# Kernel tuning notes

Measured on AMD Instinct MI355X. Metric: run time of the kernel, lower is better.

## Reference

```python
import jax, jax.numpy as jnp
import numpy as np

N_EMBD = 1024
N_HEAD = 16
HEAD_DIM = N_EMBD // N_HEAD


def setup_inputs() -> dict:
    key = jax.random.key(0)
    k1, k2, k3 = jax.random.split(key, 3)
    B, T, C = 2, 2048, N_EMBD
    x = jax.random.normal(k1, (B, T, C), dtype=jnp.float32)
    # torch nn.Linear(n_embd, 3*n_embd): weight [3C, C], bias [3C]
    W = jax.random.normal(k2, (3 * C, C), dtype=jnp.float32) * (1.0 / np.sqrt(C))
    b = jax.random.normal(k3, (3 * C,), dtype=jnp.float32) * 0.01
    return {"x": x, "W": W, "b": b}


def reference(x, W, b):
    B, T, C = x.shape
    H, D = N_HEAD, HEAD_DIM
    qkv = jnp.einsum('btc,oc->bto', x, W) + b          # [B,T,3C]
    q, k, v = jnp.split(qkv, 3, axis=2)
    # [B,H,T,D]
    q = q.reshape(B, T, H, D).transpose(0, 2, 1, 3)
    k = k.reshape(B, T, H, D).transpose(0, 2, 1, 3)
    v = v.reshape(B, T, H, D).transpose(0, 2, 1, 3)
    scale = 1.0 / np.sqrt(D).astype(np.float32)
    scores = jnp.einsum('bhid,bhjd->bhij', q, k) * scale   # [B,H,T,T]
    causal = jnp.tril(jnp.ones((T, T), dtype=bool))
    w = jnp.where(causal, jax.nn.relu(scores), 0.0)        # ReLU, no softmax
    y = jnp.einsum('bhij,bhjd->bhid', w, v)                # [B,H,T,D]
    return y.transpose(0, 2, 1, 3).reshape(B, T, C)
```

## Files before the change

### kernel.cpp

```cpp
#include <hip/hip_runtime.h>

typedef __bf16 bf16;
typedef __bf16 bf16x8 __attribute__((ext_vector_type(8)));
typedef float  f32x4  __attribute__((ext_vector_type(4)));

#define T_SEQ   2048
#define D_HEAD  64
#define NH      16
#define BH      32
#define C_EMB   1024
#define WS_STRIDE (BH * T_SEQ * D_HEAD)
#define XN (4096 * 1024)
#define WN (3072 * 1024)
#define WS_NEEDED ((size_t)(3 * WS_STRIDE + XN + WN) * 2)
#define CVT_GRID 3584

__device__ __forceinline__ bf16x8 cvt8(float4 a, float4 b) {
    bf16x8 r;
    r[0] = (__bf16)a.x; r[1] = (__bf16)a.y; r[2] = (__bf16)a.z; r[3] = (__bf16)a.w;
    r[4] = (__bf16)b.x; r[5] = (__bf16)b.y; r[6] = (__bf16)b.z; r[7] = (__bf16)b.w;
    return r;
}

__device__ __forceinline__ void gl_lds16(const bf16* g, bf16* l) {
    __builtin_amdgcn_global_load_lds(
        (const __attribute__((address_space(1))) unsigned int*)g,
        (__attribute__((address_space(3))) unsigned int*)l,
        16, 0, 0);
}

__device__ __forceinline__ unsigned pack_bf16(float a, float b) {
    union { __bf16 h[2]; unsigned u; } pk;
    pk.h[0] = (__bf16)a; pk.h[1] = (__bf16)b;
    return pk.u;
}

__global__ __launch_bounds__(256) void cvt_bf16(
    const float* __restrict__ x, const float* __restrict__ W,
    bf16* __restrict__ xb, bf16* __restrict__ wb)
{
    const int t = blockIdx.x * 256 + threadIdx.x;
    const float* src; bf16* dst; int base;
    if (t < XN / 8) { src = x; dst = xb; base = t * 8; }
    else           { src = W; dst = wb; base = (t - XN / 8) * 8; }
    float4 a = *(const float4*)(src + base);
    float4 b = *(const float4*)(src + base + 4);
    *(bf16x8*)(dst + base) = cvt8(a, b);
}

#define LDA(d, qi) {                                                          \
    const bf16* abase_ = Sh + (d)*16384 + (qi)*8192 + (wm*64 + l15)*64;       \
    _Pragma("unroll")                                                         \
    for (int ii_ = 0; ii_ < 4; ii_++) {                                       \
        _Pragma("unroll")                                                     \
        for (int dk_ = 0; dk_ < 2; dk_++)                                     \
            aF[ii_][dk_] = *(const bf16x8*)(abase_ + ii_*1024                 \
                                            + (((dk_*4 + l4) ^ k7) * 8));     \
    }                                                                         \
}

#define LDB(d, qj, bFv) {                                                     \
    const bf16* bbase_ = Sh + 32768 + (d)*16384 + (qj)*8192                   \
                         + (wn*32 + l15)*64;                                  \
    _Pragma("unroll")                                                         \
    for (int jj_ = 0; jj_ < 2; jj_++) {                                       \
        _Pragma("unroll")                                                     \
        for (int dk_ = 0; dk_ < 2; dk_++)                                     \
            bFv[jj_][dk_] = *(const bf16x8*)(bbase_ + jj_*1024                \
                                             + (((dk_*4 + l4) ^ k7) * 8));    \
    }                                                                         \
}

#define STA(d, qi, s, ko) gl_lds16(                                           \
    aSrc + (size_t)((qi)*64 + (s)*128) * 1024 + (ko),                         \
    Sh + (d)*16384 + (qi)*8192 + (s)*4096 + w*512)

#define STB(d, qj, s, ko) gl_lds16(                                           \
    bSrc + (size_t)((s)*128 + (qj)*32) * 1024 + (ko),                         \
    Sh + 32768 + (d)*16384 + (qj)*8192 + (s)*4096 + w*512)

#define MMAQ(qi, qj, bFv) {                                                   \
    __builtin_amdgcn_s_setprio(1);                                            \
    _Pragma("unroll")                                                         \
    for (int dk_ = 0; dk_ < 2; dk_++) {                                       \
        _Pragma("unroll")                                                     \
        for (int ii_ = 0; ii_ < 4; ii_++) {                                   \
            _Pragma("unroll")                                                 \
            for (int jj_ = 0; jj_ < 2; jj_++)                                 \
                acc[(qi)*4 + ii_][(qj)*2 + jj_] =                             \
                    __builtin_amdgcn_mfma_f32_16x16x32_bf16(                  \
                        aF[ii_][dk_], bFv[jj_][dk_],                          \
                        acc[(qi)*4 + ii_][(qj)*2 + jj_], 0, 0, 0);            \
        }                                                                     \
    }                                                                         \
    __builtin_amdgcn_s_setprio(0);                                            \
}

#define BAR   __builtin_amdgcn_s_barrier()
#define LGKM0 asm volatile("s_waitcnt lgkmcnt(0)" ::: "memory")

#define HALF(d, sk)                                                           \
                                                                      \
    LDA(d, 0) LDB(d, 0, bF0)                                                  \
    BAR; LGKM0;                                                               \
    MMAQ(0, 0, bF0)                                                           \
    BAR;                                                                      \
                                                                      \
    LDB(d, 1, bF1)                                                            \
    STA(d, 0, 0, sk); STA(d, 0, 1, sk); STB(d, 0, 0, sk); STB(d, 0, 1, sk);   \
    BAR; LGKM0;                                                               \
    MMAQ(0, 1, bF1)                                                           \
    BAR;                                                                      \
                                                                      \
    LDA(d, 1)                                                                 \
    STB(d, 1, 0, sk); STB(d, 1, 1, sk);                                       \
    BAR; LGKM0;                                                               \
    MMAQ(1, 0, bF0)                                                           \
    BAR;                                                                      \
                                                                      \
    STA(d, 1, 0, sk); STA(d, 1, 1, sk);                                       \
    BAR;                                                                      \
    MMAQ(1, 1, bF1)                                                           \
    asm volatile("s_waitcnt vmcnt(8)" ::: "memory");                          \
    BAR;

__global__ __launch_bounds__(512, 2) void qkv_gemm3(
    const bf16* __restrict__ xb, const bf16* __restrict__ wb,
    const float* __restrict__ bias, bf16* __restrict__ ws)
{
    __shared__ bf16 Sh[65536];

    const int tid  = threadIdx.x;
    const int lane = tid & 63;
    const int w    = tid >> 6;
    const int wm   = w >> 2, wn = w & 3;
    const int l15  = lane & 15, l4 = lane >> 4;
    const int k7   = l15 & 7;
    const int l8   = lane >> 3;
    const int csw  = (lane & 7) ^ l8;

    const int swz = (blockIdx.x & 7) * 24 + (blockIdx.x >> 3);
    const int bm  = swz / 12, bn = swz % 12;

    const bf16* aSrc = xb + (size_t)(bm * 256 + w * 8 + l8) * 1024 + csw * 8;
    const bf16* bSrc = wb + (size_t)(bn * 256 + (w >> 2) * 64 + (w & 3) * 8 + l8) * 1024
                          + csw * 8;

    f32x4 acc[8][4];
#pragma unroll
    for (int i = 0; i < 8; i++)
#pragma unroll
        for (int j = 0; j < 4; j++) acc[i][j] = (f32x4){0.f, 0.f, 0.f, 0.f};

    bf16x8 aF[4][2], bF0[2][2], bF1[2][2];

    STA(0,0,0,0);  STA(0,0,1,0);  STB(0,0,0,0);  STB(0,0,1,0);
    STB(0,1,0,0);  STB(0,1,1,0);  STA(0,1,0,0);  STA(0,1,1,0);
    STA(1,0,0,64); STA(1,0,1,64); STB(1,0,0,64); STB(1,0,1,64);
    STB(1,1,0,64); STB(1,1,1,64); STA(1,1,0,64); STA(1,1,1,64);
    asm volatile("s_waitcnt vmcnt(8)" ::: "memory");
    BAR;

    for (int it = 0; it < 8; ++it) {
        const int sk0 = (it < 7 ? (2 * it + 2) : 15) * 64;
        const int sk1 = (it < 7 ? (2 * it + 3) : 15) * 64;
        HALF(0, sk0)
        HALF(1, sk1)
    }
    asm volatile("s_waitcnt vmcnt(0)" ::: "memory");
    BAR;

    float bv[4];
#pragma unroll
    for (int j = 0; j < 4; j++) bv[j] = bias[bn * 256 + wn * 64 + j * 16 + l15];

    const int which = bn >> 2;
    const int h     = (bn & 3) * 4 + wn;
    const int bi    = bm >> 3;
    const int tBase = (bm & 7) * 256 + wm * 128;
    const float qs  = (which == 0) ? 0.125f : 1.0f;
    bf16* Wl = Sh + w * 8192;

    if (which < 2) {
#pragma unroll
        for (int i = 0; i < 8; i++)
#pragma unroll
            for (int j = 0; j < 4; j++)
#pragma unroll
                for (int r = 0; r < 4; r++) {
                    const int lm = i * 16 + l4 * 4 + r;
                    const int dd = j * 16 + l15;
                    const int cp = (dd >> 3) ^ (lm & 7);
                    Wl[lm * 64 + cp * 8 + (dd & 7)] =
                        (__bf16)((acc[i][j][r] + bv[j]) * qs);
                }
#pragma unroll
        for (int e = 0; e < 16; e++) {
            const int lm = e * 8 + l8;
            const int c  = lane & 7;
            bf16x8 v8 = *(const bf16x8*)&Wl[lm * 64 + ((c ^ (lm & 7)) * 8)];
            const int t = tBase + lm;
            *(bf16x8*)&ws[(size_t)which * WS_STRIDE
                          + ((size_t)(bi * NH + h) * T_SEQ + t) * D_HEAD + c * 8] = v8;
        }
    } else {
#pragma unroll
        for (int i = 0; i < 8; i++)
#pragma unroll
            for (int j = 0; j < 4; j++) {
                const int dd = j * 16 + l15;
#pragma unroll
                for (int p = 0; p < 2; p++) {
                    const int lm = i * 16 + l4 * 4 + 2 * p;
                    const int ch = lm >> 3;
                    const int cp = (ch & 8) | ((ch & 7) ^ (dd & 7));
                    *(unsigned*)&Wl[dd * 128 + cp * 8 + (lm & 7)] =
                        pack_bf16(acc[i][j][2 * p] + bv[j],
                                  acc[i][j][2 * p + 1] + bv[j]);
                }
            }
        bf16* vt = ws + 2 * (size_t)WS_STRIDE;
#pragma unroll
        for (int e = 0; e < 16; e++) {
            const int dd = e * 4 + l4;
            const int c  = l15;
            const int cp = (c & 8) | ((c & 7) ^ (dd & 7));
            bf16x8 v8 = *(const bf16x8*)&Wl[dd * 128 + cp * 8];
            *(bf16x8*)&vt[((size_t)(bi * NH + h) * D_HEAD + dd) * T_SEQ
                          + tBase + c * 8] = v8;
        }
    }
}

__global__ __launch_bounds__(256) void qkv_gemm(
    const float* __restrict__ x, const float* __restrict__ W,
    const float* __restrict__ bias, bf16* __restrict__ ws)
{
    __shared__ bf16 As[128 * 40];
    __shared__ bf16 Bs[128 * 40];

    const int tid  = threadIdx.x;
    const int lane = tid & 63;
    const int w    = tid >> 6;
    const int wm   = w >> 1, wn = w & 1;
    const int l15  = lane & 15, l4 = lane >> 4;
    const int bm   = blockIdx.x / 24, bn = blockIdx.x % 24;

    const int srow = tid >> 1;
    const int scol = (tid & 1) * 16;
    const float* xg = x + (size_t)(bm * 128 + srow) * 1024 + scol;
    const float* wg = W + (size_t)(bn * 128 + srow) * 1024 + scol;
    bf16* asw = &As[srow * 40 + scol];
    bf16* bsw = &Bs[srow * 40 + scol];

    f32x4 acc[4][4];
#pragma unroll
    for (int i = 0; i < 4; i++)
#pragma unroll
        for (int j = 0; j < 4; j++) acc[i][j] = (f32x4){0.f, 0.f, 0.f, 0.f};

    float bv[4];
#pragma unroll
    for (int j = 0; j < 4; j++) bv[j] = bias[bn * 128 + wn * 64 + j * 16 + l15];

    for (int kk = 0; kk < 32; ++kk) {
        const float* xp = xg + kk * 32;
        const float* wp = wg + kk * 32;
        float4 a0 = *(const float4*)(xp + 0);
        float4 a1 = *(const float4*)(xp + 4);
        float4 a2 = *(const float4*)(xp + 8);
        float4 a3 = *(const float4*)(xp + 12);
        float4 b0 = *(const float4*)(wp + 0);
        float4 b1 = *(const float4*)(wp + 4);
        float4 b2 = *(const float4*)(wp + 8);
        float4 b3 = *(const float4*)(wp + 12);

        __syncthreads();
        *(bf16x8*)(asw + 0) = cvt8(a0, a1);
        *(bf16x8*)(asw + 8) = cvt8(a2, a3);
        *(bf16x8*)(bsw + 0) = cvt8(b0, b1);
        *(bf16x8*)(bsw + 8) = cvt8(b2, b3);
        __syncthreads();

        bf16x8 aF[4], bF[4];
#pragma unroll
        for (int s = 0; s < 4; s++) {
            aF[s] = *(const bf16x8*)&As[(wm * 64 + s * 16 + l15) * 40 + l4 * 8];
            bF[s] = *(const bf16x8*)&Bs[(wn * 64 + s * 16 + l15) * 40 + l4 * 8];
        }
#pragma unroll
        for (int i = 0; i < 4; i++)
#pragma unroll
            for (int j = 0; j < 4; j++)
                acc[i][j] = __builtin_amdgcn_mfma_f32_16x16x32_bf16(
                    aF[i], bF[j], acc[i][j], 0, 0, 0);
    }

#pragma unroll
    for (int i = 0; i < 4; i++) {
#pragma unroll
        for (int j = 0; j < 4; j++) {
            const int n     = bn * 128 + wn * 64 + j * 16 + l15;
            const int which = n >> 10;
            const int cc    = n & 1023;
            const int h     = cc >> 6, d = cc & 63;
            const float qs  = (which == 0) ? 0.125f : 1.0f;
#pragma unroll
            for (int r = 0; r < 4; r++) {
                const int m  = bm * 128 + wm * 64 + i * 16 + l4 * 4 + r;
                const int bi = m >> 11, t = m & 2047;
                const int bh = bi * NH + h;
                const float v = (acc[i][j][r] + bv[j]) * qs;
                size_t idx;
                if (which == 2)
                    idx = 2 * (size_t)WS_STRIDE + ((size_t)bh * D_HEAD + d) * T_SEQ + t;
                else
                    idx = (size_t)which * WS_STRIDE + ((size_t)bh * T_SEQ + t) * D_HEAD + d;
                ws[idx] = (__bf16)v;
            }
        }
    }
}

__global__ __launch_bounds__(256) void attn(
    const bf16* __restrict__ ws, float* __restrict__ out)
{
    __shared__ bf16 Ks[128 * 64];
    __shared__ bf16 Vts[64 * 128];

    const int tid  = threadIdx.x;
    const int lane = tid & 63;
    const int w    = tid >> 6;
    const int l15  = lane & 15, qd = lane >> 4;

    const int bh = blockIdx.x & 31;
    const int u  = blockIdx.x >> 5;
    const int qt = (u < 8) ? u : (23 - u);
    const int nj = qt + 1;
    const int qb = qt * 128;

    const bf16* qg = ws + (size_t)bh * (T_SEQ * D_HEAD);
    const bf16* kg = ws + WS_STRIDE + (size_t)bh * (T_SEQ * D_HEAD);
    const bf16* vt = ws + 2 * (size_t)WS_STRIDE + (size_t)bh * (D_HEAD * T_SEQ);
    const int b = bh >> 4, h = bh & 15;

    const int ksub = lane >> 3;
    const int kc   = lane & 7;
    const int vsub = qd;
    const int vc   = l15;

    bf16x8 qF[2][2];
#pragma unroll
    for (int sm = 0; sm < 2; sm++)
#pragma unroll
        for (int dk = 0; dk < 2; dk++)
            qF[sm][dk] = *(const bf16x8*)(qg
                + (qb + w * 32 + sm * 16 + l15) * 64 + dk * 32 + qd * 8);

    f32x4 o[2][4];
#pragma unroll
    for (int sm = 0; sm < 2; sm++)
#pragma unroll
        for (int sd = 0; sd < 4; sd++) o[sm][sd] = (f32x4){0.f, 0.f, 0.f, 0.f};

    for (int jt = 0; jt < nj; ++jt) {
        __syncthreads();
#pragma unroll
        for (int e = 0; e < 4; e++) {
            const int rb = w * 32 + e * 8;
            gl_lds16(kg + (size_t)(jt * 128 + rb + ksub) * 64 + ((kc ^ ksub) * 8),
                     &Ks[rb * 64]);
        }
#pragma unroll
        for (int e = 0; e < 4; e++) {
            const int rb = w * 16 + e * 4;
            const int sw = (rb & 12) + vsub;
            gl_lds16(vt + (size_t)(rb + vsub) * T_SEQ + jt * 128 + ((vc ^ sw) * 8),
                     &Vts[rb * 128]);
        }
        __syncthreads();

        const bool need_mask = (jt == nj - 1);
        unsigned PK[2][8][2];
#pragma unroll
        for (int kn = 0; kn < 8; kn++) {
            const int r7  = 4 * (kn & 1) + (l15 & 3);
            const int row = 32 * (kn >> 1) + 8 * (l15 >> 2) + r7;
            bf16x8 kf0 = *(const bf16x8*)&Ks[row * 64 + ((qd ^ r7) * 8)];
            bf16x8 kf1 = *(const bf16x8*)&Ks[row * 64 + (((4 + qd) ^ r7) * 8)];
            f32x4 s0 = {0.f, 0.f, 0.f, 0.f}, s1 = {0.f, 0.f, 0.f, 0.f};
            s0 = __builtin_amdgcn_mfma_f32_16x16x32_bf16(kf0, qF[0][0], s0, 0, 0, 0);
            s0 = __builtin_amdgcn_mfma_f32_16x16x32_bf16(kf1, qF[0][1], s0, 0, 0, 0);
            s1 = __builtin_amdgcn_mfma_f32_16x16x32_bf16(kf0, qF[1][0], s1, 0, 0, 0);
            s1 = __builtin_amdgcn_mfma_f32_16x16x32_bf16(kf1, qF[1][1], s1, 0, 0, 0);
            const int keyb = jt * 128 + 32 * (kn >> 1) + 8 * qd + 4 * (kn & 1);
#pragma unroll
            for (int sm = 0; sm < 2; sm++) {
                const f32x4 sv = sm ? s1 : s0;
                const int q = qb + w * 32 + sm * 16 + l15;
                float v[4];
#pragma unroll
                for (int r = 0; r < 4; r++) {
                    float val = fmaxf(sv[r], 0.f);
                    if (need_mask && q < keyb + r) val = 0.f;
                    v[r] = val;
                }
                PK[sm][kn][0] = pack_bf16(v[0], v[1]);
                PK[sm][kn][1] = pack_bf16(v[2], v[3]);
            }
        }

#pragma unroll
        for (int kk = 0; kk < 4; kk++) {
            bf16x8 pF[2];
#pragma unroll
            for (int sm = 0; sm < 2; sm++) {
                union { unsigned dw[4]; bf16x8 v; } uu;
                uu.dw[0] = PK[sm][2 * kk + 0][0];
                uu.dw[1] = PK[sm][2 * kk + 0][1];
                uu.dw[2] = PK[sm][2 * kk + 1][0];
                uu.dw[3] = PK[sm][2 * kk + 1][1];
                pF[sm] = uu.v;
            }
#pragma unroll
            for (int sd = 0; sd < 4; sd++) {
                bf16x8 vf = *(const bf16x8*)&Vts[(sd * 16 + l15) * 128
                                                 + (((kk * 4 + qd) ^ l15) * 8)];
                o[0][sd] = __builtin_amdgcn_mfma_f32_16x16x32_bf16(pF[0], vf, o[0][sd], 0, 0, 0);
                o[1][sd] = __builtin_amdgcn_mfma_f32_16x16x32_bf16(pF[1], vf, o[1][sd], 0, 0, 0);
            }
        }
    }

#pragma unroll
    for (int sm = 0; sm < 2; sm++)
#pragma unroll
        for (int sd = 0; sd < 4; sd++) {
            const int d = sd * 16 + l15;
#pragma unroll
            for (int r = 0; r < 4; r++) {
                const int t = qb + w * 32 + sm * 16 + qd * 4 + r;
                out[((size_t)b * T_SEQ + t) * C_EMB + h * 64 + d] = o[sm][sd][r];
            }
        }
}

extern "C" void kernel_launch(void* const* d_in, const int* in_sizes, int n_in,
                              void* d_out, int out_size, void* d_ws, size_t ws_size,
                              hipStream_t stream) {
    const float* x    = (const float*)d_in[0];
    const float* W    = (const float*)d_in[1];
    const float* bias = (const float*)d_in[2];
    float* out        = (float*)d_out;
    bf16*  ws         = (bf16*)d_ws;

    if (ws_size >= WS_NEEDED) {
        bf16* xb = ws + 3 * (size_t)WS_STRIDE;
        bf16* wb = xb + XN;
        cvt_bf16<<<dim3(CVT_GRID), dim3(256), 0, stream>>>(x, W, xb, wb);
        qkv_gemm3<<<dim3(192), dim3(512), 0, stream>>>(xb, wb, bias, ws);
    } else {
        qkv_gemm<<<dim3(768), dim3(256), 0, stream>>>(x, W, bias, ws);
    }
    attn<<<dim3(512), dim3(256), 0, stream>>>(ws, out);
}
```

Baseline: 148.1 us.

## Double-buffer K/V tiles in attention and raise MFMA wave priority

The attention kernel now keeps two LDS buffers for the K and V^T tiles and issues the direct-to-LDS loads for the next key tile before computing on the current one, using vmcnt waits and barriers. This overlaps global-memory latency with MFMA work instead of stalling at each iteration. It also wraps the MFMA sequences in s_setprio and moves the causal-mask check out of the unmasked path. LDS use doubles to 64 KB per block, which may lower occupancy. Correctness depends on the hand-written vmcnt(8) count matching the eight loads issued per stage.

```diff
diff --git a/kernel.cpp b/kernel.cpp
--- a/kernel.cpp
+++ b/kernel.cpp
@@ -322,11 +322,29 @@
     }
 }
 
+#define ASTAGE(jt_, p_) {                                                     \
+    _Pragma("unroll")                                                         \
+    for (int e_ = 0; e_ < 4; e_++) {                                          \
+        const int rb_ = w * 32 + e_ * 8;                                      \
+        gl_lds16(kg + (size_t)((jt_) * 128 + rb_ + ksub) * 64                 \
+                    + ((kc ^ ksub) * 8),                                      \
+                 &Ks[p_][rb_ * 64]);                                          \
+    }                                                                         \
+    _Pragma("unroll")                                                         \
+    for (int e_ = 0; e_ < 4; e_++) {                                          \
+        const int rb_ = w * 16 + e_ * 4;                                      \
+        const int sw_ = (rb_ & 12) + vsub;                                    \
+        gl_lds16(vt + (size_t)(rb_ + vsub) * T_SEQ + (jt_) * 128              \
+                    + ((vc ^ sw_) * 8),                                       \
+                 &Vts[p_][rb_ * 128]);                                        \
+    }                                                                         \
+}
+
 __global__ __launch_bounds__(256) void attn(
     const bf16* __restrict__ ws, float* __restrict__ out)
 {
-    __shared__ bf16 Ks[128 * 64];
-    __shared__ bf16 Vts[64 * 128];
+    __shared__ bf16 Ks[2][128 * 64];
+    __shared__ bf16 Vts[2][64 * 128];
 
     const int tid  = threadIdx.x;
     const int lane = tid & 63;
@@ -363,22 +381,20 @@
 #pragma unroll
         for (int sd = 0; sd < 4; sd++) o[sm][sd] = (f32x4){0.f, 0.f, 0.f, 0.f};
 
+    ASTAGE(0, 0);
+
     for (int jt = 0; jt < nj; ++jt) {
-        __syncthreads();
-#pragma unroll
-        for (int e = 0; e < 4; e++) {
-            const int rb = w * 32 + e * 8;
-            gl_lds16(kg + (size_t)(jt * 128 + rb + ksub) * 64 + ((kc ^ ksub) * 8),
-                     &Ks[rb * 64]);
-        }
-#pragma unroll
-        for (int e = 0; e < 4; e++) {
-            const int rb = w * 16 + e * 4;
-            const int sw = (rb & 12) + vsub;
-            gl_lds16(vt + (size_t)(rb + vsub) * T_SEQ + jt * 128 + ((vc ^ sw) * 8),
-                     &Vts[rb * 128]);
-        }
-        __syncthreads();
+        const int p = jt & 1;
+        if (jt + 1 < nj) {
+            ASTAGE(jt + 1, p ^ 1);
+            asm volatile("s_waitcnt vmcnt(8)" ::: "memory");
+        } else {
+            asm volatile("s_waitcnt vmcnt(0)" ::: "memory");
+        }
+        BAR;
+
+        const bf16* Kp = Ks[p];
+        const bf16* Vp = Vts[p];
 
         const bool need_mask = (jt == nj - 1);
         unsigned PK[2][8][2];
@@ -386,24 +402,27 @@
         for (int kn = 0; kn < 8; kn++) {
             const int r7  = 4 * (kn & 1) + (l15 & 3);
             const int row = 32 * (kn >> 1) + 8 * (l15 >> 2) + r7;
-            bf16x8 kf0 = *(const bf16x8*)&Ks[row * 64 + ((qd ^ r7) * 8)];
-            bf16x8 kf1 = *(const bf16x8*)&Ks[row * 64 + (((4 + qd) ^ r7) * 8)];
+            bf16x8 kf0 = *(const bf16x8*)&Kp[row * 64 + ((qd ^ r7) * 8)];
+            bf16x8 kf1 = *(const bf16x8*)&Kp[row * 64 + (((4 + qd) ^ r7) * 8)];
             f32x4 s0 = {0.f, 0.f, 0.f, 0.f}, s1 = {0.f, 0.f, 0.f, 0.f};
+            __builtin_amdgcn_s_setprio(1);
             s0 = __builtin_amdgcn_mfma_f32_16x16x32_bf16(kf0, qF[0][0], s0, 0, 0, 0);
             s0 = __builtin_amdgcn_mfma_f32_16x16x32_bf16(kf1, qF[0][1], s0, 0, 0, 0);
             s1 = __builtin_amdgcn_mfma_f32_16x16x32_bf16(kf0, qF[1][0], s1, 0, 0, 0);
             s1 = __builtin_amdgcn_mfma_f32_16x16x32_bf16(kf1, qF[1][1], s1, 0, 0, 0);
+            __builtin_amdgcn_s_setprio(0);
             const int keyb = jt * 128 + 32 * (kn >> 1) + 8 * qd + 4 * (kn & 1);
 #pragma unroll
             for (int sm = 0; sm < 2; sm++) {
                 const f32x4 sv = sm ? s1 : s0;
-                const int q = qb + w * 32 + sm * 16 + l15;
                 float v[4];
 #pragma unroll
-                for (int r = 0; r < 4; r++) {
-                    float val = fmaxf(sv[r], 0.f);
-                    if (need_mask && q < keyb + r) val = 0.f;
-                    v[r] = val;
+                for (int r = 0; r < 4; r++) v[r] = fmaxf(sv[r], 0.f);
+                if (need_mask) {
+                    const int q = qb + w * 32 + sm * 16 + l15;
+#pragma unroll
+                    for (int r = 0; r < 4; r++)
+                        if (q < keyb + r) v[r] = 0.f;
                 }
                 PK[sm][kn][0] = pack_bf16(v[0], v[1]);
                 PK[sm][kn][1] = pack_bf16(v[2], v[3]);
@@ -422,14 +441,18 @@
                 uu.dw[3] = PK[sm][2 * kk + 1][1];
                 pF[sm] = uu.v;
             }
+            __builtin_amdgcn_s_setprio(1);
 #pragma unroll
             for (int sd = 0; sd < 4; sd++) {
-                bf16x8 vf = *(const bf16x8*)&Vts[(sd * 16 + l15) * 128
-                                                 + (((kk * 4 + qd) ^ l15) * 8)];
+                bf16x8 vf = *(const bf16x8*)&Vp[(sd * 16 + l15) * 128
+                                                + (((kk * 4 + qd) ^ l15) * 8)];
                 o[0][sd] = __builtin_amdgcn_mfma_f32_16x16x32_bf16(pF[0], vf, o[0][sd], 0, 0, 0);
                 o[1][sd] = __builtin_amdgcn_mfma_f32_16x16x32_bf16(pF[1], vf, o[1][sd], 0, 0, 0);
             }
-        }
+            __builtin_amdgcn_s_setprio(0);
+        }
+
+        BAR;
     }
 
 #pragma unroll
```

Result: no change. 146.7 us (-1.0%).
